# Kernel tuning notes

Hardware: AMD Instinct MI355X
Metric: run time of the kernel (lower is better)

## Reference

```python
import jax, jax.numpy as jnp
import numpy as np

B, T, D, H, F, E, K = 4, 1024, 1024, 16, 2048, 8, 2
LN_EPS = 1e-6  # flax LayerNorm default


def setup_inputs() -> dict:
    key = jax.random.key(0)
    ks = jax.random.split(key, 8)
    s = 0.02
    return {
        "x": jax.random.normal(ks[0], (B, T, D), jnp.float32),
        "ln1_scale": jnp.ones((D,), jnp.float32),
        "ln1_bias": jnp.zeros((D,), jnp.float32),
        "qkv_w": jax.random.normal(ks[1], (D, 3 * D), jnp.float32) * s,
        "qkv_b": jnp.zeros((3 * D,), jnp.float32),
        "out_w": jax.random.normal(ks[2], (D, D), jnp.float32) * s,
        "out_b": jnp.zeros((D,), jnp.float32),
        "ln2_scale": jnp.ones((D,), jnp.float32),
        "ln2_bias": jnp.zeros((D,), jnp.float32),
        "router_w": jax.random.normal(ks[3], (D, E), jnp.float32) * s,
        "w1": jax.random.normal(ks[4], (E, D, F), jnp.float32) * s,
        "b1": jnp.zeros((E, F), jnp.float32),
        "w2": jax.random.normal(ks[5], (E, F, D), jnp.float32) * s,
        "b2": jnp.zeros((E, D), jnp.float32),
    }


def _layernorm(x, scale, bias):
    mu = jnp.mean(x, axis=-1, keepdims=True)
    var = jnp.mean(jnp.square(x - mu), axis=-1, keepdims=True)
    return (x - mu) * jax.lax.rsqrt(var + LN_EPS) * scale + bias


def _attention(x, qkv_w, qkv_b, out_w, out_b):
    b, t, d = x.shape
    hd = d // H
    qkv = x @ qkv_w + qkv_b
    q, k, v = jnp.split(qkv, 3, axis=-1)
    q = q.reshape(b, t, H, hd).transpose(0, 2, 1, 3)  # (B,H,T,hd)
    k = k.reshape(b, t, H, hd).transpose(0, 2, 1, 3)
    v = v.reshape(b, t, H, hd).transpose(0, 2, 1, 3)
    scale = jnp.sqrt(jnp.float32(hd))
    scores = jnp.einsum("bhqd,bhkd->bhqk", q, k) / scale
    causal = jnp.triu(jnp.ones((t, t), jnp.bool_), k=1)
    scores = jnp.where(causal[None, None], -1e9, scores)
    attn = jax.nn.softmax(scores, axis=-1)
    out = jnp.einsum("bhqk,bhkd->bhqd", attn, v)
    out = out.transpose(0, 2, 1, 3).reshape(b, t, d)
    return out @ out_w + out_b


def _moe(x, router_w, w1, b1, w2, b2):
    b, t, d = x.shape
    logits = x @ router_w  # (B,T,E)
    probs = jax.nn.softmax(logits, axis=-1)
    topk_vals, topk_idx = jax.lax.top_k(logits, K)  # (B,T,K)
    gates = jax.nn.softmax(topk_vals, axis=-1)
    # aux load-balancing loss from top-1 dispatch
    dispatch = jax.nn.one_hot(topk_idx[..., 0], E, dtype=x.dtype)
    f = jnp.mean(dispatch, axis=(0, 1))
    P = jnp.mean(probs, axis=(0, 1))
    aux_loss = E * jnp.sum(f * P)
    # dense all-expert compute (faithful to original)
    h = jax.nn.gelu(jnp.einsum("btd,edf->ebtf", x, w1) + b1[:, None, None, :])
    eo = jnp.einsum("ebtf,efd->ebtd", h, w2) + b2[:, None, None, :]  # (E,B,T,D)
    bi = jnp.arange(b)[:, None, None]
    ti = jnp.arange(t)[None, :, None]
    selected = eo[topk_idx, bi, ti, :]  # (B,T,K,D)
    out = jnp.sum(gates[..., None] * selected, axis=2)
    return out, aux_loss


def reference(x, ln1_scale, ln1_bias, qkv_w, qkv_b, out_w, out_b,
              ln2_scale, ln2_bias, router_w, w1, b1, w2, b2):
    res = x
    h = _layernorm(x, ln1_scale, ln1_bias)
    h = _attention(h, qkv_w, qkv_b, out_w, out_b)
    x = h + res
    res = x
    hn = _layernorm(x, ln2_scale, ln2_bias)
    moe_out, aux_loss = _moe(hn, router_w, w1, b1, w2, b2)
    return moe_out + res, aux_loss
```

## Files before the change

kernel.cpp:

```cpp
#include <hip/hip_runtime.h>
#include <hip/hip_bf16.h>

using bf16 = __hip_bfloat16;
typedef __attribute__((ext_vector_type(8))) short short8;
typedef __attribute__((ext_vector_type(4))) float f32x4;

__device__ __forceinline__ unsigned short f2bu(float x) {
  union { bf16 b; unsigned short u; } cv; cv.b = __float2bfloat16(x); return cv.u;
}

__device__ __forceinline__ void gload_lds16(const bf16* g, bf16* l) {
  __builtin_amdgcn_global_load_lds(
      (const __attribute__((address_space(1))) void*)g,
      (__attribute__((address_space(3))) void*)l, 16, 0, 0);
}

__global__ __launch_bounds__(256) void transpose_to_bf16(
    const float* __restrict__ in, bf16* __restrict__ out, int R, int C) {
  __shared__ float tile[32][33];
  size_t batch_off = (size_t)blockIdx.z * R * C;
  in += batch_off; out += batch_off;
  int c0 = blockIdx.x * 32, r0 = blockIdx.y * 32;
  int tx = threadIdx.x & 31, ty = threadIdx.x >> 5;
#pragma unroll
  for (int i = 0; i < 32; i += 8)
    tile[ty + i][tx] = in[(size_t)(r0 + ty + i) * C + c0 + tx];
  __syncthreads();
#pragma unroll
  for (int i = 0; i < 32; i += 8)
    out[(size_t)(c0 + ty + i) * R + r0 + tx] = __float2bfloat16(tile[tx][ty + i]);
}

__global__ __launch_bounds__(256) void ln_kernel(
    const float* __restrict__ in, const float* __restrict__ sc,
    const float* __restrict__ bi, bf16* __restrict__ out) {
  int row = blockIdx.x, tid = threadIdx.x;
  const float4* xr = (const float4*)(in + (size_t)row * 1024);
  float4 v = xr[tid];
  float s = v.x + v.y + v.z + v.w;
  float sq = v.x * v.x + v.y * v.y + v.z * v.z + v.w * v.w;
#pragma unroll
  for (int m = 1; m < 64; m <<= 1) { s += __shfl_xor(s, m); sq += __shfl_xor(sq, m); }
  __shared__ float red[8];
  int wid = tid >> 6, lane = tid & 63;
  if (lane == 0) { red[wid] = s; red[4 + wid] = sq; }
  __syncthreads();
  s = red[0] + red[1] + red[2] + red[3];
  sq = red[4] + red[5] + red[6] + red[7];
  float mu = s * (1.f / 1024.f);
  float rstd = rsqrtf(sq * (1.f / 1024.f) - mu * mu + 1e-6f);
  float4 scv = ((const float4*)sc)[tid];
  float4 biv = ((const float4*)bi)[tid];
  ushort4 ov;
  ov.x = f2bu((v.x - mu) * rstd * scv.x + biv.x);
  ov.y = f2bu((v.y - mu) * rstd * scv.y + biv.y);
  ov.z = f2bu((v.z - mu) * rstd * scv.z + biv.z);
  ov.w = f2bu((v.w - mu) * rstd * scv.w + biv.w);
  ((ushort4*)(out + (size_t)row * 1024))[tid] = ov;
}

template <int EPI, bool GATHER, bool GROUPED>
__global__ __launch_bounds__(256) void gemm_bt(
    const bf16* __restrict__ A, const bf16* __restrict__ B,
    const float* __restrict__ bias, const float* __restrict__ resid,
    void* __restrict__ C, bf16* __restrict__ VT, const int* __restrict__ gidx,
    const int* __restrict__ counts, const int* __restrict__ offsets,
    int M, int N, int K) {
  int e = blockIdx.z;
  int Mcnt = M, base = 0;
  if (GROUPED) { Mcnt = counts[e]; base = offsets[e]; }
  int m0 = blockIdx.y * 128, n0 = blockIdx.x * 128;
  if (m0 >= Mcnt) return;
  const bf16* Bp = B + (size_t)e * N * K;
  const float* biasp = bias + (size_t)e * N;
  __shared__ __align__(16) bf16 As[2][128 * 64];
  __shared__ __align__(16) bf16 Bs[2][128 * 64];
  int tid = threadIdx.x, lane = tid & 63, wid = tid >> 6;
  int lr = lane & 15, lg = lane >> 4;
  int wr = (wid >> 1) * 64, wc = (wid & 1) * 64;
  const bf16* aptr[4];
  const bf16* bptr[4];
  int dsto[4];
#pragma unroll
  for (int i = 0; i < 4; ++i) {
    int idx = i * 256 + tid;
    int r = idx >> 3, cb = idx & 7;
    int cbs = cb ^ (r & 7);
    int gr = m0 + r;
    int cl = gr < Mcnt ? gr : (Mcnt - 1);
    size_t arow = GATHER ? (size_t)gidx[base + cl] : (size_t)(base + cl);
    aptr[i] = A + arow * K + cbs * 8;
    bptr[i] = Bp + (size_t)(n0 + r) * K + cbs * 8;
    dsto[i] = idx * 8;
  }
  int xa = lr & 7;
  int colk[2];
  colk[0] = (lg ^ xa) * 8;
  colk[1] = ((lg + 4) ^ xa) * 8;
  int arow_lds[4], brow_lds[4];
#pragma unroll
  for (int m_ = 0; m_ < 4; ++m_) arow_lds[m_] = (wr + m_ * 16 + lr) * 64;
#pragma unroll
  for (int n_ = 0; n_ < 4; ++n_) brow_lds[n_] = (wc + n_ * 16 + lr) * 64;

  f32x4 acc[4][4] = {};
  int nt = K >> 6;
#pragma unroll
  for (int i = 0; i < 4; ++i) {
    gload_lds16(aptr[i], &As[0][dsto[i]]);
    gload_lds16(bptr[i], &Bs[0][dsto[i]]);
  }
  __syncthreads();
  for (int t = 0; t < nt; ++t) {
    int cur = t & 1;
    if (t + 1 < nt) {
      int k0 = (t + 1) << 6;
#pragma unroll
      for (int i = 0; i < 4; ++i) {
        gload_lds16(aptr[i] + k0, &As[cur ^ 1][dsto[i]]);
        gload_lds16(bptr[i] + k0, &Bs[cur ^ 1][dsto[i]]);
      }
    }
#pragma unroll
    for (int h = 0; h < 2; ++h) {
      short8 af[4], bfg[4];
#pragma unroll
      for (int m_ = 0; m_ < 4; ++m_)
        af[m_] = *(const short8*)&As[cur][arow_lds[m_] + colk[h]];
#pragma unroll
      for (int n_ = 0; n_ < 4; ++n_)
        bfg[n_] = *(const short8*)&Bs[cur][brow_lds[n_] + colk[h]];
#pragma unroll
      for (int m_ = 0; m_ < 4; ++m_)
#pragma unroll
        for (int n_ = 0; n_ < 4; ++n_)
          acc[m_][n_] = __builtin_amdgcn_mfma_f32_16x16x32_bf16(af[m_], bfg[n_], acc[m_][n_], 0, 0, 0);
    }
    __syncthreads();
  }
#pragma unroll
  for (int n_ = 0; n_ < 4; ++n_) {
    int acol = n0 + wc + n_ * 16 + lr;
    float bv = biasp[acol];
#pragma unroll
    for (int m_ = 0; m_ < 4; ++m_) {
      int rbase = m0 + wr + m_ * 16 + lg * 4;
#pragma unroll
      for (int q = 0; q < 4; ++q) {
        int gr = rbase + q;
        if (gr >= Mcnt) continue;
        size_t crow = (size_t)(base + gr);
        float v = acc[m_][n_][q] + bv;
        if (EPI == 1) {
          float z = 0.7978845608028654f * (v + 0.044715f * v * v * v);
          float t2 = __expf(2.f * z);
          v = v * (t2 / (t2 + 1.f));
          ((bf16*)C)[crow * N + acol] = __float2bfloat16(v);
        } else if (EPI == 2) {
          ((float*)C)[crow * N + acol] = v + resid[crow * N + acol];
        } else if (EPI == 3) {
          if (acol < 2048) {
            ((bf16*)C)[crow * N + acol] = __float2bfloat16(v);
          } else {
            int dg = acol - 2048;
            int hh = dg >> 6, dd = dg & 63;
            int bb = (int)(crow >> 10), tt = (int)(crow & 1023);
            VT[(((size_t)bb * 16 + hh) * 64 + dd) * 1024 + tt] = __float2bfloat16(v);
          }
        } else {
          ((bf16*)C)[crow * N + acol] = __float2bfloat16(v);
        }
      }
    }
  }
}

__global__ __launch_bounds__(256) void attn_kernel(const bf16* __restrict__ qkv,
                                                   const bf16* __restrict__ vt,
                                                   bf16* __restrict__ out) {
  constexpr int T = 1024, QS = 3072;
  int bh = blockIdx.y;
  int b = bh >> 4, h = bh & 15;
  __shared__ __align__(16) bf16 Ks[64][72];
  __shared__ __align__(16) bf16 Vs[64][72];
  __shared__ __align__(16) bf16 Pl[4][16][72];
  int tid = threadIdx.x, lane = tid & 63, wid = tid >> 6;
  int lr = lane & 15, lg = lane >> 4;
  const size_t rowb = (size_t)b * T;
  const float SC = 0.18033688011112042f;
  int sr[2], scb[2];
  const bf16* kbase[2];
  const bf16* vbase[2];
#pragma unroll
  for (int i = 0; i < 2; ++i) {
    int idx = tid + i * 256;
    sr[i] = idx >> 3; scb[i] = idx & 7;
    kbase[i] = qkv + (rowb + sr[i]) * QS + 1024 + h * 64 + scb[i] * 8;
    vbase[i] = vt + ((size_t)bh * 64 + sr[i]) * T + scb[i] * 8;
  }
  for (int half = 0; half < 2; ++half) {
    int qt = (half == 0) ? blockIdx.x : (15 - blockIdx.x);
    int qrow0 = qt * 64 + wid * 16 + lg * 4;
    const bf16* qp = qkv + (rowb + qt * 64 + wid * 16 + lr) * QS + h * 64;
    short8 qf0 = *(const short8*)(qp + lg * 8);
    short8 qf1 = *(const short8*)(qp + 32 + lg * 8);
    f32x4 o[4] = {};
    float mrow[4] = {-3e38f, -3e38f, -3e38f, -3e38f};
    float lrow[4] = {0.f, 0.f, 0.f, 0.f};
    short8 kreg[2], vreg[2];
#pragma unroll
    for (int i = 0; i < 2; ++i) {
      kreg[i] = *(const short8*)kbase[i];
      vreg[i] = *(const short8*)vbase[i];
    }
    for (int kv = 0; kv <= qt; ++kv) {
      __syncthreads();
#pragma unroll
      for (int i = 0; i < 2; ++i) {
        *(short8*)&Ks[sr[i]][scb[i] * 8] = kreg[i];
        *(short8*)&Vs[sr[i]][scb[i] * 8] = vreg[i];
      }
      __syncthreads();
      if (kv < qt) {
#pragma unroll
        for (int i = 0; i < 2; ++i) {
          kreg[i] = *(const short8*)(kbase[i] + (size_t)(kv + 1) * 64 * QS);
          vreg[i] = *(const short8*)(vbase[i] + (kv + 1) * 64);
        }
      }
      f32x4 s[4];
#pragma unroll
      for (int nf = 0; nf < 4; ++nf) {
        f32x4 z = {0.f, 0.f, 0.f, 0.f};
        short8 k0 = *(const short8*)&Ks[nf * 16 + lr][lg * 8];
        short8 k1 = *(const short8*)&Ks[nf * 16 + lr][32 + lg * 8];
        z = __builtin_amdgcn_mfma_f32_16x16x32_bf16(qf0, k0, z, 0, 0, 0);
        z = __builtin_amdgcn_mfma_f32_16x16x32_bf16(qf1, k1, z, 0, 0, 0);
        s[nf] = z;
      }
      bool diag = (kv == qt);
#pragma unroll
      for (int nf = 0; nf < 4; ++nf)
#pragma unroll
        for (int q = 0; q < 4; ++q) {
          float v = s[nf][q] * SC;
          if (diag) { int key = kv * 64 + nf * 16 + lr; if (key > qrow0 + q) v = -1e9f; }
          s[nf][q] = v;
        }
      float rs[4], resc[4];
#pragma unroll
      for (int q = 0; q < 4; ++q) {
        float v = fmaxf(fmaxf(s[0][q], s[1][q]), fmaxf(s[2][q], s[3][q]));
        v = fmaxf(v, __shfl_xor(v, 1));
        v = fmaxf(v, __shfl_xor(v, 2));
        v = fmaxf(v, __shfl_xor(v, 4));
        v = fmaxf(v, __shfl_xor(v, 8));
        float mn = fmaxf(mrow[q], v);
        resc[q] = __builtin_amdgcn_exp2f(mrow[q] - mn);
        mrow[q] = mn;
        rs[q] = 0.f;
      }
#pragma unroll
      for (int nf = 0; nf < 4; ++nf)
#pragma unroll
        for (int q = 0; q < 4; ++q) {
          float p = __builtin_amdgcn_exp2f(s[nf][q] - mrow[q]);
          rs[q] += p;
          Pl[wid][lg * 4 + q][nf * 16 + lr] = __float2bfloat16(p);
        }
#pragma unroll
      for (int q = 0; q < 4; ++q) {
        float v = rs[q];
        v += __shfl_xor(v, 1); v += __shfl_xor(v, 2);
        v += __shfl_xor(v, 4); v += __shfl_xor(v, 8);
        lrow[q] = lrow[q] * resc[q] + v;
        o[0][q] *= resc[q]; o[1][q] *= resc[q]; o[2][q] *= resc[q]; o[3][q] *= resc[q];
      }
      short8 pa0 = *(const short8*)&Pl[wid][lr][lg * 8];
      short8 pa1 = *(const short8*)&Pl[wid][lr][32 + lg * 8];
#pragma unroll
      for (int nf = 0; nf < 4; ++nf) {
        short8 v0 = *(const short8*)&Vs[nf * 16 + lr][lg * 8];
        short8 v1 = *(const short8*)&Vs[nf * 16 + lr][32 + lg * 8];
        o[nf] = __builtin_amdgcn_mfma_f32_16x16x32_bf16(pa0, v0, o[nf], 0, 0, 0);
        o[nf] = __builtin_amdgcn_mfma_f32_16x16x32_bf16(pa1, v1, o[nf], 0, 0, 0);
      }
    }
#pragma unroll
    for (int q = 0; q < 4; ++q) {
      float inv = 1.0f / lrow[q];
      size_t row = rowb + qrow0 + q;
#pragma unroll
      for (int nf = 0; nf < 4; ++nf)
        out[row * 1024 + h * 64 + nf * 16 + lr] = __float2bfloat16(o[nf][q] * inv);
    }
  }
}

__global__ __launch_bounds__(64) void router_kernel(
    const float* __restrict__ x2, const float* __restrict__ sc,
    const float* __restrict__ bi, const float* __restrict__ rw,
    float* __restrict__ probs, int* __restrict__ topk, float* __restrict__ gates) {
  int t = blockIdx.x, lane = threadIdx.x;
  const float* xr = x2 + (size_t)t * 1024;
  float xv[16];
  float s = 0.f, sq = 0.f;
#pragma unroll
  for (int i = 0; i < 4; ++i) {
    float4 v = ((const float4*)xr)[lane * 4 + i];
    xv[i * 4 + 0] = v.x; xv[i * 4 + 1] = v.y; xv[i * 4 + 2] = v.z; xv[i * 4 + 3] = v.w;
    s += v.x + v.y + v.z + v.w;
    sq += v.x * v.x + v.y * v.y + v.z * v.z + v.w * v.w;
  }
#pragma unroll
  for (int m = 1; m < 64; m <<= 1) { s += __shfl_xor(s, m); sq += __shfl_xor(sq, m); }
  float mu = s * (1.f / 1024.f);
  float rstd = rsqrtf(sq * (1.f / 1024.f) - mu * mu + 1e-6f);
  float a8[8] = {};
#pragma unroll
  for (int i = 0; i < 16; ++i) {
    int d = lane * 16 + i;
    float y = (xv[i] - mu) * rstd * sc[d] + bi[d];
    const float4* rr = (const float4*)(rw + (size_t)d * 8);
    float4 r0 = rr[0], r1 = rr[1];
    a8[0] += y * r0.x; a8[1] += y * r0.y; a8[2] += y * r0.z; a8[3] += y * r0.w;
    a8[4] += y * r1.x; a8[5] += y * r1.y; a8[6] += y * r1.z; a8[7] += y * r1.w;
  }
#pragma unroll
  for (int m = 1; m < 64; m <<= 1)
#pragma unroll
    for (int e = 0; e < 8; ++e) a8[e] += __shfl_xor(a8[e], m);
  if (lane == 0) {
    float mx = a8[0];
#pragma unroll
    for (int e = 1; e < 8; ++e) mx = fmaxf(mx, a8[e]);
    float ps = 0.f, pe[8];
#pragma unroll
    for (int e = 0; e < 8; ++e) { pe[e] = expf(a8[e] - mx); ps += pe[e]; }
    float inv = 1.f / ps;
#pragma unroll
    for (int e = 0; e < 8; ++e) probs[t * 8 + e] = pe[e] * inv;
    int i0 = 0; float v0 = a8[0];
#pragma unroll
    for (int e = 1; e < 8; ++e) if (a8[e] > v0) { v0 = a8[e]; i0 = e; }
    int i1 = -1; float v1 = -3e38f;
#pragma unroll
    for (int e = 0; e < 8; ++e) if (e != i0 && a8[e] > v1) { v1 = a8[e]; i1 = e; }
    float g1 = 1.f / (1.f + expf(v0 - v1));
    topk[t * 2] = i0; topk[t * 2 + 1] = i1;
    gates[t * 2] = 1.f - g1; gates[t * 2 + 1] = g1;
  }
}

__global__ void count_kernel(const int* __restrict__ topk, int* __restrict__ counts,
                             int* __restrict__ offsets) {
  __shared__ int c[8];
  int tid = threadIdx.x;
  if (tid < 8) c[tid] = 0;
  __syncthreads();
  for (int p = tid; p < 8192; p += 256) atomicAdd(&c[topk[p]], 1);
  __syncthreads();
  if (tid == 0) {
    int off = 0;
    for (int e = 0; e < 8; ++e) { counts[e] = c[e]; offsets[e] = off; off += c[e]; }
  }
}

__global__ __launch_bounds__(256) void assign_kernel(
    const int* __restrict__ topk, const int* __restrict__ offsets,
    int* __restrict__ rows_tok, int* __restrict__ pair_pos) {
  int e = blockIdx.x;
  int tid = threadIdx.x, lane = tid & 63, wid = tid >> 6;
  int base = offsets[e];
  __shared__ int wsum[4];
  int run = 0;
  for (int start = 0; start < 8192; start += 256) {
    int p = start + tid;
    int f = (topk[p] == e) ? 1 : 0;
    int v = f;
#pragma unroll
    for (int o_ = 1; o_ < 64; o_ <<= 1) { int u = __shfl_up(v, o_); if (lane >= o_) v += u; }
    if (lane == 63) wsum[wid] = v;
    __syncthreads();
    int wbase = 0;
#pragma unroll
    for (int w = 0; w < 4; ++w) if (w < wid) wbase += wsum[w];
    int tot = wsum[0] + wsum[1] + wsum[2] + wsum[3];
    if (f) {
      int pos = base + run + wbase + v - 1;
      rows_tok[pos] = p >> 1;
      pair_pos[p] = pos;
    }
    run += tot;
    __syncthreads();
  }
}

__global__ __launch_bounds__(256) void combine_kernel(
    const float* __restrict__ x2, const bf16* __restrict__ eo,
    const float* __restrict__ gates, const int* __restrict__ pair_pos,
    float* __restrict__ out) {
  int t = blockIdx.x, tid = threadIdx.x;
  float g0 = gates[t * 2], g1 = gates[t * 2 + 1];
  size_t p0 = (size_t)pair_pos[t * 2] * 1024, p1 = (size_t)pair_pos[t * 2 + 1] * 1024;
  size_t rb = (size_t)t * 1024;
#pragma unroll
  for (int i = 0; i < 4; ++i) {
    int d = tid + i * 256;
    out[rb + d] = x2[rb + d] + g0 * __bfloat162float(eo[p0 + d]) + g1 * __bfloat162float(eo[p1 + d]);
  }
}

__global__ __launch_bounds__(256) void aux_kernel(const float* __restrict__ probs,
                                                  const int* __restrict__ topk,
                                                  float* __restrict__ out) {
  int tid = threadIdx.x, lane = tid & 63, wid = tid >> 6;
  float P[8] = {}, Fc[8] = {};
  for (int t = tid; t < 4096; t += 256) {
#pragma unroll
    for (int e = 0; e < 8; ++e) P[e] += probs[t * 8 + e];
    Fc[topk[t * 2]] += 1.f;
  }
#pragma unroll
  for (int m = 1; m < 64; m <<= 1)
#pragma unroll
    for (int e = 0; e < 8; ++e) { P[e] += __shfl_xor(P[e], m); Fc[e] += __shfl_xor(Fc[e], m); }
  __shared__ float sP[4][8], sF[4][8];
  if (lane == 0)
#pragma unroll
    for (int e = 0; e < 8; ++e) { sP[wid][e] = P[e]; sF[wid][e] = Fc[e]; }
  __syncthreads();
  if (tid == 0) {
    float aux = 0.f;
    for (int e = 0; e < 8; ++e) {
      float p = (sP[0][e] + sP[1][e] + sP[2][e] + sP[3][e]) * (1.f / 4096.f);
      float f = (sF[0][e] + sF[1][e] + sF[2][e] + sF[3][e]) * (1.f / 4096.f);
      aux += f * p;
    }
    out[0] = 8.f * aux;
  }
}

extern "C" void kernel_launch(void* const* d_in, const int* in_sizes, int n_in,
                              void* d_out, int out_size, void* d_ws, size_t ws_size,
                              hipStream_t stream) {
  (void)in_sizes; (void)n_in; (void)out_size; (void)ws_size;
  const float* x    = (const float*)d_in[0];
  const float* ln1s = (const float*)d_in[1];
  const float* ln1b = (const float*)d_in[2];
  const float* qkvw = (const float*)d_in[3];
  const float* qkvb = (const float*)d_in[4];
  const float* outw = (const float*)d_in[5];
  const float* outb = (const float*)d_in[6];
  const float* ln2s = (const float*)d_in[7];
  const float* ln2b = (const float*)d_in[8];
  const float* rw   = (const float*)d_in[9];
  const float* w1   = (const float*)d_in[10];
  const float* b1   = (const float*)d_in[11];
  const float* w2   = (const float*)d_in[12];
  const float* b2   = (const float*)d_in[13];

  char* ws = (char*)d_ws;
  size_t off = 0;
  auto alloc = [&](size_t bytes) -> char* {
    char* p = ws + off; off += (bytes + 255) & ~(size_t)255; return p;
  };
  bf16* qkvw_t  = (bf16*)alloc(3072ull * 1024 * 2);
  bf16* outw_t  = (bf16*)alloc(1024ull * 1024 * 2);
  bf16* w1_t    = (bf16*)alloc(8ull * 2048 * 1024 * 2);
  bf16* w2_t    = (bf16*)alloc(8ull * 1024 * 2048 * 2);
  bf16* h1      = (bf16*)alloc(4096ull * 1024 * 2);
  bf16* qkv     = (bf16*)alloc(4096ull * 3072 * 2);
  bf16* vtb     = (bf16*)alloc(64ull * 64 * 1024 * 2);
  bf16* attn_o  = (bf16*)alloc(4096ull * 1024 * 2);
  float* x2     = (float*)alloc(4096ull * 1024 * 4);
  bf16* ln2h    = (bf16*)alloc(4096ull * 1024 * 2);
  float* probs  = (float*)alloc(4096ull * 8 * 4);
  float* gates  = (float*)alloc(4096ull * 2 * 4);
  int* topk     = (int*)alloc(8192 * 4);
  int* counts   = (int*)alloc(64 * 4);
  int* offsets  = (int*)alloc(64 * 4);
  int* rows_tok = (int*)alloc(8192 * 4);
  int* pair_pos = (int*)alloc(8192 * 4);
  bf16* h_buf   = (bf16*)alloc(8192ull * 2048 * 2);
  bf16* eo      = (bf16*)alloc(8192ull * 1024 * 2);

  transpose_to_bf16<<<dim3(3072 / 32, 1024 / 32, 1), 256, 0, stream>>>(qkvw, qkvw_t, 1024, 3072);
  transpose_to_bf16<<<dim3(1024 / 32, 1024 / 32, 1), 256, 0, stream>>>(outw, outw_t, 1024, 1024);
  transpose_to_bf16<<<dim3(2048 / 32, 1024 / 32, 8), 256, 0, stream>>>(w1, w1_t, 1024, 2048);
  transpose_to_bf16<<<dim3(1024 / 32, 2048 / 32, 8), 256, 0, stream>>>(w2, w2_t, 2048, 1024);

  ln_kernel<<<4096, 256, 0, stream>>>(x, ln1s, ln1b, h1);

  gemm_bt<3, false, false><<<dim3(3072 / 128, 4096 / 128, 1), 256, 0, stream>>>(
      h1, qkvw_t, qkvb, nullptr, qkv, vtb, nullptr, nullptr, nullptr, 4096, 3072, 1024);

  attn_kernel<<<dim3(8, 64), 256, 0, stream>>>(qkv, vtb, attn_o);

  gemm_bt<2, false, false><<<dim3(1024 / 128, 4096 / 128, 1), 256, 0, stream>>>(
      attn_o, outw_t, outb, x, x2, nullptr, nullptr, nullptr, nullptr, 4096, 1024, 1024);

  ln_kernel<<<4096, 256, 0, stream>>>(x2, ln2s, ln2b, ln2h);

  router_kernel<<<4096, 64, 0, stream>>>(x2, ln2s, ln2b, rw, probs, topk, gates);

  count_kernel<<<1, 256, 0, stream>>>(topk, counts, offsets);
  assign_kernel<<<8, 256, 0, stream>>>(topk, offsets, rows_tok, pair_pos);

  gemm_bt<1, true, true><<<dim3(2048 / 128, 64, 8), 256, 0, stream>>>(
      ln2h, w1_t, b1, nullptr, h_buf, nullptr, rows_tok, counts, offsets, 8192, 2048, 1024);

  gemm_bt<0, false, true><<<dim3(1024 / 128, 64, 8), 256, 0, stream>>>(
      h_buf, w2_t, b2, nullptr, eo, nullptr, nullptr, counts, offsets, 8192, 1024, 2048);

  combine_kernel<<<4096, 256, 0, stream>>>(x2, eo, gates, pair_pos, (float*)d_out);
  aux_kernel<<<1, 256, 0, stream>>>(probs, topk, (float*)d_out + 4194304);
}
```

Measured before the change: 433.4 us.

## Give each wave private LDS tiles to remove block barriers in the GEMM

Rewrites the bf16 GEMM so each wave stages its own 64x64 A and B slices into a private double-buffered LDS region. Completion is tracked per wave with explicit vmcnt/lgkmcnt waits instead of block-wide __syncthreads, and the loads for tile t+2 are issued right after tile t's fragments are consumed. The aim is to remove inter-wave barrier stalls and keep loads in flight longer. In exchange, waves that share rows or columns now load them separately, which doubles global/L2 traffic, and the 128 KB LDS allocation limits each CU to one block.

```diff
diff --git a/kernel.cpp b/kernel.cpp
--- a/kernel.cpp
+++ b/kernel.cpp
@@ -60,7 +60,7 @@
 }
 
 template <int EPI, bool GATHER, bool GROUPED>
-__global__ __launch_bounds__(256) void gemm_bt(
+__global__ __launch_bounds__(256) void gemm_ws(
     const bf16* __restrict__ A, const bf16* __restrict__ B,
     const float* __restrict__ bias, const float* __restrict__ resid,
     void* __restrict__ C, bf16* __restrict__ VT, const int* __restrict__ gidx,
@@ -73,75 +73,80 @@
   if (m0 >= Mcnt) return;
   const bf16* Bp = B + (size_t)e * N * K;
   const float* biasp = bias + (size_t)e * N;
-  __shared__ __align__(16) bf16 As[2][128 * 64];
-  __shared__ __align__(16) bf16 Bs[2][128 * 64];
+  __shared__ __align__(16) bf16 smem[65536];
   int tid = threadIdx.x, lane = tid & 63, wid = tid >> 6;
   int lr = lane & 15, lg = lane >> 4;
   int wr = (wid >> 1) * 64, wc = (wid & 1) * 64;
-  const bf16* aptr[4];
-  const bf16* bptr[4];
-  int dsto[4];
-#pragma unroll
-  for (int i = 0; i < 4; ++i) {
-    int idx = i * 256 + tid;
-    int r = idx >> 3, cb = idx & 7;
-    int cbs = cb ^ (r & 7);
-    int gr = m0 + r;
+  bf16* wbase = smem + wid * 16384;
+  const bf16* ap[8];
+  const bf16* bp[8];
+  int rloc = lane >> 3, cb = lane & 7;
+#pragma unroll
+  for (int gi = 0; gi < 8; ++gi) {
+    int ra = wr + gi * 8 + rloc;
+    int gr = m0 + ra;
     int cl = gr < Mcnt ? gr : (Mcnt - 1);
     size_t arow = GATHER ? (size_t)gidx[base + cl] : (size_t)(base + cl);
-    aptr[i] = A + arow * K + cbs * 8;
-    bptr[i] = Bp + (size_t)(n0 + r) * K + cbs * 8;
-    dsto[i] = idx * 8;
-  }
+    ap[gi] = A + arow * K + (size_t)((cb ^ (ra & 7)) * 8);
+    int rb = wc + gi * 8 + rloc;
+    bp[gi] = Bp + (size_t)(n0 + rb) * K + (size_t)((cb ^ (rb & 7)) * 8);
+  }
+  int dl = lane * 8;
+  auto stage = [&](int buf, int t) {
+    bf16* da = wbase + buf * 8192;
+    bf16* db = da + 4096;
+#pragma unroll
+    for (int gi = 0; gi < 8; ++gi)
+      gload_lds16(ap[gi] + (size_t)t * 64, da + gi * 512 + dl);
+#pragma unroll
+    for (int gi = 0; gi < 8; ++gi)
+      gload_lds16(bp[gi] + (size_t)t * 64, db + gi * 512 + dl);
+  };
   int xa = lr & 7;
   int colk[2];
   colk[0] = (lg ^ xa) * 8;
   colk[1] = ((lg + 4) ^ xa) * 8;
-  int arow_lds[4], brow_lds[4];
-#pragma unroll
-  for (int m_ = 0; m_ < 4; ++m_) arow_lds[m_] = (wr + m_ * 16 + lr) * 64;
-#pragma unroll
-  for (int n_ = 0; n_ < 4; ++n_) brow_lds[n_] = (wc + n_ * 16 + lr) * 64;
-
   f32x4 acc[4][4] = {};
   int nt = K >> 6;
-#pragma unroll
-  for (int i = 0; i < 4; ++i) {
-    gload_lds16(aptr[i], &As[0][dsto[i]]);
-    gload_lds16(bptr[i], &Bs[0][dsto[i]]);
-  }
-  __syncthreads();
+  stage(0, 0);
+  stage(1, 1);
   for (int t = 0; t < nt; ++t) {
-    int cur = t & 1;
     if (t + 1 < nt) {
-      int k0 = (t + 1) << 6;
-#pragma unroll
-      for (int i = 0; i < 4; ++i) {
-        gload_lds16(aptr[i] + k0, &As[cur ^ 1][dsto[i]]);
-        gload_lds16(bptr[i] + k0, &Bs[cur ^ 1][dsto[i]]);
-      }
-    }
-#pragma unroll
-    for (int h = 0; h < 2; ++h) {
-      short8 af[4], bfg[4];
+      asm volatile("s_waitcnt vmcnt(16)" ::: "memory");
+    } else {
+      asm volatile("s_waitcnt vmcnt(0)" ::: "memory");
+    }
+    __builtin_amdgcn_sched_barrier(0);
+    const bf16* la = wbase + (t & 1) * 8192;
+    const bf16* lb = la + 4096;
+    short8 af[4][2], bfg[4][2];
+#pragma unroll
+    for (int m_ = 0; m_ < 4; ++m_)
+#pragma unroll
+      for (int h = 0; h < 2; ++h)
+        af[m_][h] = *(const short8*)&la[(m_ * 16 + lr) * 64 + colk[h]];
+#pragma unroll
+    for (int n_ = 0; n_ < 4; ++n_)
+#pragma unroll
+      for (int h = 0; h < 2; ++h)
+        bfg[n_][h] = *(const short8*)&lb[(n_ * 16 + lr) * 64 + colk[h]];
+#pragma unroll
+    for (int h = 0; h < 2; ++h)
 #pragma unroll
       for (int m_ = 0; m_ < 4; ++m_)
-        af[m_] = *(const short8*)&As[cur][arow_lds[m_] + colk[h]];
-#pragma unroll
-      for (int n_ = 0; n_ < 4; ++n_)
-        bfg[n_] = *(const short8*)&Bs[cur][brow_lds[n_] + colk[h]];
-#pragma unroll
-      for (int m_ = 0; m_ < 4; ++m_)
 #pragma unroll
         for (int n_ = 0; n_ < 4; ++n_)
-          acc[m_][n_] = __builtin_amdgcn_mfma_f32_16x16x32_bf16(af[m_], bfg[n_], acc[m_][n_], 0, 0, 0);
-    }
-    __syncthreads();
+          acc[m_][n_] = __builtin_amdgcn_mfma_f32_16x16x32_bf16(af[m_][h], bfg[n_][h], acc[m_][n_], 0, 0, 0);
+    if (t + 2 < nt) {
+      asm volatile("s_waitcnt lgkmcnt(0)" ::: "memory");
+      __builtin_amdgcn_sched_barrier(0);
+      stage(t & 1, t + 2);
+    }
   }
 #pragma unroll
   for (int n_ = 0; n_ < 4; ++n_) {
     int acol = n0 + wc + n_ * 16 + lr;
-    float bv = biasp[acol];
+    float bvs = biasp[acol];
 #pragma unroll
     for (int m_ = 0; m_ < 4; ++m_) {
       int rbase = m0 + wr + m_ * 16 + lg * 4;
@@ -150,11 +155,11 @@
         int gr = rbase + q;
         if (gr >= Mcnt) continue;
         size_t crow = (size_t)(base + gr);
-        float v = acc[m_][n_][q] + bv;
+        float v = acc[m_][n_][q] + bvs;
         if (EPI == 1) {
           float z = 0.7978845608028654f * (v + 0.044715f * v * v * v);
-          float t2 = __expf(2.f * z);
-          v = v * (t2 / (t2 + 1.f));
+          float ez = __expf(2.f * z);
+          v = v * (ez / (ez + 1.f));
           ((bf16*)C)[crow * N + acol] = __float2bfloat16(v);
         } else if (EPI == 2) {
           ((float*)C)[crow * N + acol] = v + resid[crow * N + acol];
@@ -492,12 +497,12 @@
 
   ln_kernel<<<4096, 256, 0, stream>>>(x, ln1s, ln1b, h1);
 
-  gemm_bt<3, false, false><<<dim3(3072 / 128, 4096 / 128, 1), 256, 0, stream>>>(
+  gemm_ws<3, false, false><<<dim3(3072 / 128, 4096 / 128, 1), 256, 0, stream>>>(
       h1, qkvw_t, qkvb, nullptr, qkv, vtb, nullptr, nullptr, nullptr, 4096, 3072, 1024);
 
   attn_kernel<<<dim3(8, 64), 256, 0, stream>>>(qkv, vtb, attn_o);
 
-  gemm_bt<2, false, false><<<dim3(1024 / 128, 4096 / 128, 1), 256, 0, stream>>>(
+  gemm_ws<2, false, false><<<dim3(1024 / 128, 4096 / 128, 1), 256, 0, stream>>>(
       attn_o, outw_t, outb, x, x2, nullptr, nullptr, nullptr, nullptr, 4096, 1024, 1024);
 
   ln_kernel<<<4096, 256, 0, stream>>>(x2, ln2s, ln2b, ln2h);
@@ -507,10 +512,10 @@
   count_kernel<<<1, 256, 0, stream>>>(topk, counts, offsets);
   assign_kernel<<<8, 256, 0, stream>>>(topk, offsets, rows_tok, pair_pos);
 
-  gemm_bt<1, true, true><<<dim3(2048 / 128, 64, 8), 256, 0, stream>>>(
+  gemm_ws<1, true, true><<<dim3(2048 / 128, 8192 / 128, 8), 256, 0, stream>>>(
       ln2h, w1_t, b1, nullptr, h_buf, nullptr, rows_tok, counts, offsets, 8192, 2048, 1024);
 
-  gemm_bt<0, false, true><<<dim3(1024 / 128, 64, 8), 256, 0, stream>>>(
+  gemm_ws<0, false, true><<<dim3(1024 / 128, 8192 / 128, 8), 256, 0, stream>>>(
       h_buf, w2_t, b2, nullptr, eo, nullptr, nullptr, counts, offsets, 8192, 1024, 2048);
 
   combine_kernel<<<4096, 256, 0, stream>>>(x2, eo, gates, pair_pos, (float*)d_out);
```

Result: slower. 482.4 us (+11.3%).
